# Kernel tuning notes

Hardware: AMD Instinct MI355X
Metric: run time of the kernel (lower is better)

## Reference

```python
import jax, jax.numpy as jnp
import numpy as np

GROUPS = 8   # channels // group_size with group_size=8 for C=64
EPS = 1e-5


def group_norm_qc(x0, x1, gamma, beta):
    """LatticeGroupNorm: stats computed jointly over both cosets per (batch, group)."""
    B, C, H, W = x0.shape
    g = GROUPS
    xg = jnp.concatenate([x0.reshape(B, g, -1), x1.reshape(B, g, -1)], axis=-1)
    mean = xg.mean(axis=-1).reshape(B, g, 1, 1, 1)
    var = xg.var(axis=-1).reshape(B, g, 1, 1, 1)
    inv = jax.lax.rsqrt(var + EPS)
    ga = gamma[None, :, None, None]
    be = beta[None, :, None, None]

    def norm(x):
        xr = x.reshape(B, g, C // g, H, W)
        return ((xr - mean) * inv).reshape(B, C, H, W) * ga + be

    return norm(x0), norm(x1)


def qc_conv(x0, x1, w_center, w_corner, bias):
    """Quincunx LatticePad+LatticeConvolution with stencil
    [(0,0),(2,0),(0,2),(2,2),(1,1)], center (1,1).
    w_center: [O,I] tap (1,1) (same-coset 1x1).
    w_corner: [O,I,2,2] taps (0,0),(2,0),(0,2),(2,2) (cross-coset 2x2).
    Pad keeps output cosets the same size as inputs ('same' lattice conv)."""
    dn = ('NCHW', 'OIHW', 'NCHW')

    def c1(x):
        return jnp.einsum('oi,bihw->bohw', w_center, x)

    def c2(x, pad):
        return jax.lax.conv_general_dilated(x, w_corner, (1, 1), pad,
                                            dimension_numbers=dn)

    b = bias[None, :, None, None]
    # coset0 output gathers coset1 at (i-1+a, j-1+b) -> pad top/left
    out0 = c1(x0) + c2(x1, ((1, 0), (1, 0))) + b
    # coset1 output gathers coset0 at (i+a, j+b) -> pad bottom/right
    out1 = c1(x1) + c2(x0, ((0, 1), (0, 1))) + b
    return out0, out1


def setup_inputs() -> dict:
    key = jax.random.key(0)
    ks = jax.random.split(key, 10)
    B, C, H, W = 2, 64, 256, 256
    s = 0.05
    return {
        'x0': jax.random.normal(ks[0], (B, C, H, W), jnp.float32),
        'x1': jax.random.normal(ks[1], (B, C, H, W), jnp.float32),
        'g1': jnp.ones((C,), jnp.float32),
        'b1': jnp.zeros((C,), jnp.float32),
        'w1_center': jax.random.normal(ks[2], (C, C), jnp.float32) * s,
        'w1_corner': jax.random.normal(ks[3], (C, C, 2, 2), jnp.float32) * s,
        'bias1': jax.random.normal(ks[4], (C,), jnp.float32) * s,
        'g2': jnp.ones((C,), jnp.float32),
        'b2': jnp.zeros((C,), jnp.float32),
        'w2_center': jax.random.normal(ks[5], (C, C), jnp.float32) * s,
        'w2_corner': jax.random.normal(ks[6], (C, C, 2, 2), jnp.float32) * s,
        'bias2': jax.random.normal(ks[7], (C,), jnp.float32) * s,
        'w_skip': jax.random.normal(ks[8], (C, C), jnp.float32) * s,
        'bias_skip': jax.random.normal(ks[9], (C,), jnp.float32) * s,
        'g_skip': jnp.ones((C,), jnp.float32),
        'beta_skip': jnp.zeros((C,), jnp.float32),
    }


def reference(x0, x1, g1, b1, w1_center, w1_corner, bias1,
              g2, b2, w2_center, w2_corner, bias2,
              w_skip, bias_skip, g_skip, beta_skip):
    # conv path: GN -> ReLU -> pad+conv -> GN -> ReLU -> pad+conv
    h0, h1 = group_norm_qc(x0, x1, g1, b1)
    h0, h1 = jax.nn.relu(h0), jax.nn.relu(h1)
    h0, h1 = qc_conv(h0, h1, w1_center, w1_corner, bias1)
    h0, h1 = group_norm_qc(h0, h1, g2, b2)
    h0, h1 = jax.nn.relu(h0), jax.nn.relu(h1)
    h0, h1 = qc_conv(h0, h1, w2_center, w2_corner, bias2)
    # skip path: 1x1 lattice conv (stencil [(0,0)]) -> GN
    bsk = bias_skip[None, :, None, None]
    s0 = jnp.einsum('oi,bihw->bohw', w_skip, x0) + bsk
    s1 = jnp.einsum('oi,bihw->bohw', w_skip, x1) + bsk
    s0, s1 = group_norm_qc(s0, s1, g_skip, beta_skip)
    # residual add; stack the two cosets as leading axis for a single output
    return jnp.stack([h0 + s0, h1 + s1])
```

## Files before the change

### kernel.cpp

```cpp
#include <hip/hip_runtime.h>

typedef __attribute__((ext_vector_type(8))) __bf16 bf16x8;
typedef __attribute__((ext_vector_type(2))) __bf16 bf16x2;
typedef __attribute__((ext_vector_type(4))) float f32x4;

#define MFMA16(a,b,c) __builtin_amdgcn_mfma_f32_16x16x32_bf16(a,b,c,0,0,0)

static constexpr int HW = 65536;
static constexpr int WD = 256;
static constexpr int NB = 2;
static constexpr double INV_N = 1.0 / 1048576.0;
static constexpr float EPSV = 1e-5f;

static constexpr size_t OFF_P1  = 0;
static constexpr size_t OFF_P2  = 131072;
static constexpr size_t OFF_NRM = 196608;
static constexpr size_t OFF_A1  = 200704;
static constexpr size_t OFF_A2  = OFF_A1 + 40960;
static constexpr size_t OFF_XT  = OFF_A2 + 40960;
static constexpr size_t SZ_T    = (size_t)2 * NB * HW * 64 * 2;
static constexpr size_t OFF_S   = OFF_XT + SZ_T;
static constexpr size_t OFF_H   = OFF_S + SZ_T;

__global__ void k_prep(const float* __restrict__ wc1, const float* __restrict__ wk1,
                       const float* __restrict__ wc2, const float* __restrict__ wk2,
                       __bf16* __restrict__ A1, __bf16* __restrict__ A2) {
  const int stage = blockIdx.x;
  const float* wc = stage ? wc2 : wc1;
  const float* wk = stage ? wk2 : wk1;
  __bf16* A = stage ? A2 : A1;
  for (int idx = threadIdx.x; idx < 64 * 320; idx += blockDim.x) {
    int o = idx / 320, k = idx - o * 320;
    float v;
    if (k < 64) v = wc[o * 64 + k];
    else {
      int t = (k - 64) >> 6;
      int c = k & 63;
      v = wk[(o * 64 + c) * 4 + t];
    }
    A[idx] = (__bf16)v;
  }
}

__global__ __launch_bounds__(256) void k1(
    const float* __restrict__ x0, const float* __restrict__ x1,
    const float* __restrict__ wskip, const float* __restrict__ bskip,
    __bf16* __restrict__ xt, __bf16* __restrict__ sout, float* __restrict__ p1) {
  const int row = blockIdx.x;
  const int b   = blockIdx.y;
  const int co  = blockIdx.z;
  const float* x = co ? x1 : x0;
  __shared__ __attribute__((aligned(16))) __bf16 tile[256 * 72];
  __shared__ float redp[64];
  __shared__ float reds[16];
  const int t = threadIdx.x;
  const int wv = t >> 6, lane = t & 63;

  const float* xbase = x + (size_t)b * 64 * HW + (size_t)row * WD + t;
  __bf16* xtbase = xt + (((size_t)(co * NB + b) * HW) + (size_t)row * WD + t) * 64;

  for (int cg = 0; cg < 8; ++cg) {
    bf16x8 v;
    float sum = 0.f, sq = 0.f;
#pragma unroll
    for (int j = 0; j < 8; ++j) {
      float f = xbase[(size_t)(cg * 8 + j) * HW];
      v[j] = (__bf16)f;
      sum += f;
      sq = fmaf(f, f, sq);
    }
    *(bf16x8*)&tile[t * 72 + cg * 8] = v;
    *(bf16x8*)&xtbase[cg * 8] = v;
#pragma unroll
    for (int m = 1; m < 64; m <<= 1) {
      sum += __shfl_xor(sum, m, 64);
      sq  += __shfl_xor(sq, m, 64);
    }
    if (lane == 0) {
      redp[wv * 16 + cg] = sum;
      redp[wv * 16 + 8 + cg] = sq;
    }
  }
  __syncthreads();

  const int ln = lane & 15, q = lane >> 4;
  const int ch0 = wv * 16 + q * 4;
  bf16x8 a0, a1;
#pragma unroll
  for (int j = 0; j < 8; ++j) {
    a0[j] = (__bf16)wskip[(wv * 16 + ln) * 64 + q * 8 + j];
    a1[j] = (__bf16)wskip[(wv * 16 + ln) * 64 + 32 + q * 8 + j];
  }
  float bia[4];
#pragma unroll
  for (int r = 0; r < 4; ++r) bia[r] = bskip[ch0 + r];

  float ssum = 0.f, ssq = 0.f;
  for (int n = 0; n < 16; ++n) {
    f32x4 acc = {0.f, 0.f, 0.f, 0.f};
    bf16x8 b0 = *(const bf16x8*)&tile[(n * 16 + ln) * 72 + q * 8];
    bf16x8 b1 = *(const bf16x8*)&tile[(n * 16 + ln) * 72 + 32 + q * 8];
    acc = MFMA16(a0, b0, acc);
    acc = MFMA16(a1, b1, acc);
    float v[4];
#pragma unroll
    for (int r = 0; r < 4; ++r) {
      v[r] = acc[r] + bia[r];
      ssum += v[r];
      ssq = fmaf(v[r], v[r], ssq);
    }
    size_t sb = (((size_t)(co * NB + b) * HW) + (size_t)row * WD + n * 16 + ln) * 64 + ch0;
    bf16x2 p0; p0[0] = (__bf16)v[0]; p0[1] = (__bf16)v[1];
    bf16x2 p1v; p1v[0] = (__bf16)v[2]; p1v[1] = (__bf16)v[3];
    *(bf16x2*)&sout[sb] = p0;
    *(bf16x2*)&sout[sb + 2] = p1v;
  }
#pragma unroll
  for (int m = 1; m < 32; m <<= 1) {
    ssum += __shfl_xor(ssum, m, 64);
    ssq  += __shfl_xor(ssq, m, 64);
  }
  if (lane == 0)  { reds[2 * wv] = ssum;     reds[8 + 2 * wv] = ssq; }
  if (lane == 32) { reds[2 * wv + 1] = ssum; reds[8 + 2 * wv + 1] = ssq; }

  __syncthreads();
  if (t < 32) {
    float val;
    if (t < 16) val = redp[t] + redp[16 + t] + redp[32 + t] + redp[48 + t];
    else val = reds[t - 16];
    const int bf1 = (co * 2 + b) * 256 + row;
    p1[(size_t)bf1 * 32 + t] = val;
  }
}

__global__ __launch_bounds__(256) void k_r1(
    const float* __restrict__ p1, const float* __restrict__ g1, const float* __restrict__ be1,
    const float* __restrict__ gsk, const float* __restrict__ besk, float* __restrict__ nrm) {
  const int t = threadIdx.x;
  __shared__ double red[64];
  const int sid = t >> 2, sub = t & 3;
  const int which = sid >> 5, b = (sid >> 4) & 1, kg = sid & 15;
  const int col = which * 16 + kg;
  double v = 0.0;
  for (int j = sub; j < 512; j += 4) {
    int co = j >> 8, rr = j & 255;
    v += (double)p1[((size_t)(co * 2 + b) * 256 + rr) * 32 + col];
  }
  v += __shfl_xor(v, 1, 64);
  v += __shfl_xor(v, 2, 64);
  if (sub == 0) red[sid] = v;
  __syncthreads();
  {
    int half = t >> 7;
    int b2 = (t >> 6) & 1, ch = t & 63, g = ch >> 3;
    int base = half * 32 + b2 * 16;
    double mean = red[base + g] * INV_N;
    double var  = red[base + 8 + g] * INV_N - mean * mean;
    float inv  = rsqrtf((float)var + EPSV);
    float ga = half ? gsk[ch] : g1[ch];
    float be = half ? besk[ch] : be1[ch];
    float sc = inv * ga;
    nrm[half * 256 + b2 * 128 + ch] = sc;
    nrm[half * 256 + b2 * 128 + 64 + ch] = be - (float)mean * sc;
  }
}

__global__ __launch_bounds__(256) void k2(
    const __bf16* __restrict__ xt, const __bf16* __restrict__ A1,
    const float* __restrict__ nrm, const float* __restrict__ bias1,
    __bf16* __restrict__ h, float* __restrict__ p2) {
  const int tx = blockIdx.x & 15, ty = blockIdx.x >> 4;
  const int b = blockIdx.y;
  const int y0p = ty * 8, x0p = tx * 16;
  __shared__ __attribute__((aligned(16))) __bf16 tl[2][153 * 72];
  __shared__ float sc[64], sh[64];
  __shared__ float lst[16];
  const int t = threadIdx.x;

  if (t < 64) {
    sc[t] = nrm[b * 128 + t];
    sh[t] = nrm[b * 128 + 64 + t];
  }
  if (t < 16) lst[t] = 0.f;
  __syncthreads();

  for (int u = t; u < 2 * 153 * 8; u += 256) {
    int cs = u / 1224;
    int rr = u - cs * 1224;
    int px = rr >> 3, cg = rr & 7;
    int ly = px / 17, lx = px - ly * 17;
    int gy = y0p + ly - cs, gx = x0p + lx - cs;
    bf16x8 v;
#pragma unroll
    for (int j = 0; j < 8; ++j) v[j] = (__bf16)0.f;
    if ((unsigned)gy < 256u && (unsigned)gx < 256u) {
      bf16x8 raw = *(const bf16x8*)&xt[(((size_t)(cs * NB + b) * WD + gy) * WD + gx) * 64 + cg * 8];
#pragma unroll
      for (int j = 0; j < 8; ++j) {
        float f = fmaf((float)raw[j], sc[cg * 8 + j], sh[cg * 8 + j]);
        v[j] = (__bf16)fmaxf(f, 0.f);
      }
    }
    *(bf16x8*)&tl[cs][px * 72 + cg * 8] = v;
  }
  __syncthreads();

  const int wv = t >> 6, lane = t & 63, ln = lane & 15, q = lane >> 4;
  const int co = wv & 1, mh = wv >> 1;
  const int q8 = q * 8;
  bf16x8 af[2][10];
#pragma unroll
  for (int m = 0; m < 2; ++m)
#pragma unroll
    for (int kk = 0; kk < 10; ++kk)
      af[m][kk] = *(const bf16x8*)&A1[(mh * 32 + m * 16 + ln) * 320 + kk * 32 + q8];

  f32x4 acc[8][2];
#pragma unroll
  for (int n = 0; n < 8; ++n)
#pragma unroll
    for (int m = 0; m < 2; ++m) acc[n][m] = (f32x4){0.f, 0.f, 0.f, 0.f};

  const __bf16* tc = tl[co];
  const __bf16* to = tl[1 - co];
#pragma unroll
  for (int n = 0; n < 8; ++n) {
    const int cpix = co ? ((n + 1) * 17 + ln + 1) : (n * 17 + ln);
    const int tb = n * 17 + ln;
    const __bf16* pc = tc + cpix * 72 + q8;
    const __bf16* p0 = to + tb * 72 + q8;
    const __bf16* p1p = to + (tb + 1) * 72 + q8;
    const __bf16* p2p = to + (tb + 17) * 72 + q8;
    const __bf16* p3 = to + (tb + 18) * 72 + q8;
    bf16x8 bb;
    bb = *(const bf16x8*)pc;         acc[n][0]=MFMA16(af[0][0],bb,acc[n][0]); acc[n][1]=MFMA16(af[1][0],bb,acc[n][1]);
    bb = *(const bf16x8*)(pc + 32);  acc[n][0]=MFMA16(af[0][1],bb,acc[n][0]); acc[n][1]=MFMA16(af[1][1],bb,acc[n][1]);
    bb = *(const bf16x8*)p0;         acc[n][0]=MFMA16(af[0][2],bb,acc[n][0]); acc[n][1]=MFMA16(af[1][2],bb,acc[n][1]);
    bb = *(const bf16x8*)(p0 + 32);  acc[n][0]=MFMA16(af[0][3],bb,acc[n][0]); acc[n][1]=MFMA16(af[1][3],bb,acc[n][1]);
    bb = *(const bf16x8*)p1p;        acc[n][0]=MFMA16(af[0][4],bb,acc[n][0]); acc[n][1]=MFMA16(af[1][4],bb,acc[n][1]);
    bb = *(const bf16x8*)(p1p + 32); acc[n][0]=MFMA16(af[0][5],bb,acc[n][0]); acc[n][1]=MFMA16(af[1][5],bb,acc[n][1]);
    bb = *(const bf16x8*)p2p;        acc[n][0]=MFMA16(af[0][6],bb,acc[n][0]); acc[n][1]=MFMA16(af[1][6],bb,acc[n][1]);
    bb = *(const bf16x8*)(p2p + 32); acc[n][0]=MFMA16(af[0][7],bb,acc[n][0]); acc[n][1]=MFMA16(af[1][7],bb,acc[n][1]);
    bb = *(const bf16x8*)p3;         acc[n][0]=MFMA16(af[0][8],bb,acc[n][0]); acc[n][1]=MFMA16(af[1][8],bb,acc[n][1]);
    bb = *(const bf16x8*)(p3 + 32);  acc[n][0]=MFMA16(af[0][9],bb,acc[n][0]); acc[n][1]=MFMA16(af[1][9],bb,acc[n][1]);
  }

  float s2s[2] = {0.f, 0.f}, s2q[2] = {0.f, 0.f};
  float bia[2][4];
#pragma unroll
  for (int m = 0; m < 2; ++m)
#pragma unroll
    for (int r = 0; r < 4; ++r) bia[m][r] = bias1[mh * 32 + m * 16 + q * 4 + r];

#pragma unroll
  for (int n = 0; n < 8; ++n) {
    int gy = y0p + n;
#pragma unroll
    for (int m = 0; m < 2; ++m) {
      int ch0 = mh * 32 + m * 16 + q * 4;
      size_t hb = (((size_t)(co * NB + b) * WD + gy) * WD + x0p + ln) * 64 + ch0;
      float v[4];
#pragma unroll
      for (int r = 0; r < 4; ++r) {
        v[r] = acc[n][m][r] + bia[m][r];
        s2s[m] += v[r];
        s2q[m] = fmaf(v[r], v[r], s2q[m]);
      }
      bf16x2 p0; p0[0] = (__bf16)v[0]; p0[1] = (__bf16)v[1];
      bf16x2 p1v; p1v[0] = (__bf16)v[2]; p1v[1] = (__bf16)v[3];
      *(bf16x2*)&h[hb] = p0;
      *(bf16x2*)&h[hb + 2] = p1v;
    }
  }
#pragma unroll
  for (int m = 0; m < 2; ++m) {
    float a_ = s2s[m], c_ = s2q[m];
#pragma unroll
    for (int mk = 1; mk < 32; mk <<= 1) {
      a_ += __shfl_xor(a_, mk, 64);
      c_ += __shfl_xor(c_, mk, 64);
    }
    if ((lane & 31) == 0) {
      int g = mh * 4 + m * 2 + (q >> 1);
      atomicAdd(&lst[g], a_);
      atomicAdd(&lst[8 + g], c_);
    }
  }
  __syncthreads();
  if (t < 16) p2[((size_t)b * 512 + blockIdx.x) * 16 + t] = lst[t];
}

__global__ __launch_bounds__(256) void k_r2(
    const float* __restrict__ p2, const float* __restrict__ g2, const float* __restrict__ be2,
    float* __restrict__ nrm) {
  const int t = threadIdx.x;
  __shared__ double red[32];
  const int sid = t >> 3, sub = t & 7;
  const int b = sid >> 4, col = sid & 15;
  double v = 0.0;
  for (int j = sub; j < 512; j += 8)
    v += (double)p2[((size_t)b * 512 + j) * 16 + col];
  v += __shfl_xor(v, 1, 64);
  v += __shfl_xor(v, 2, 64);
  v += __shfl_xor(v, 4, 64);
  if (sub == 0) red[sid] = v;
  __syncthreads();
  if (t < 128) {
    int b2 = t >> 6, ch = t & 63, g = ch >> 3;
    double mean = red[b2 * 16 + g] * INV_N;
    double var  = red[b2 * 16 + 8 + g] * INV_N - mean * mean;
    float inv  = rsqrtf((float)var + EPSV);
    float sc = inv * g2[ch];
    nrm[512 + b2 * 128 + ch] = sc;
    nrm[512 + b2 * 128 + 64 + ch] = be2[ch] - (float)mean * sc;
  }
}

__global__ __launch_bounds__(256) void k3(
    const __bf16* __restrict__ hin, const __bf16* __restrict__ A2,
    const float* __restrict__ nrm, const float* __restrict__ bias2,
    const __bf16* __restrict__ sin_, float* __restrict__ out) {
  const int tx = blockIdx.x & 15, ty = blockIdx.x >> 4;
  const int b = blockIdx.y;
  const int y0p = ty * 8, x0p = tx * 16;
  __shared__ __attribute__((aligned(16))) __bf16 tl[2][153 * 72];
  __shared__ float sc2[64], sh2[64], scS[64], shS[64];
  const int t = threadIdx.x;

  if (t < 64) {
    sc2[t] = nrm[512 + b * 128 + t];
    sh2[t] = nrm[512 + b * 128 + 64 + t];
    scS[t] = nrm[256 + b * 128 + t];
    shS[t] = nrm[256 + b * 128 + 64 + t];
  }
  __syncthreads();

  for (int u = t; u < 2 * 153 * 8; u += 256) {
    int cs = u / 1224;
    int rr = u - cs * 1224;
    int px = rr >> 3, cg = rr & 7;
    int ly = px / 17, lx = px - ly * 17;
    int gy = y0p + ly - cs, gx = x0p + lx - cs;
    bf16x8 v;
#pragma unroll
    for (int j = 0; j < 8; ++j) v[j] = (__bf16)0.f;
    if ((unsigned)gy < 256u && (unsigned)gx < 256u) {
      bf16x8 raw = *(const bf16x8*)&hin[(((size_t)(cs * NB + b) * WD + gy) * WD + gx) * 64 + cg * 8];
#pragma unroll
      for (int j = 0; j < 8; ++j) {
        float f = fmaf((float)raw[j], sc2[cg * 8 + j], sh2[cg * 8 + j]);
        v[j] = (__bf16)fmaxf(f, 0.f);
      }
    }
    *(bf16x8*)&tl[cs][px * 72 + cg * 8] = v;
  }
  __syncthreads();

  const int wv = t >> 6, lane = t & 63, ln = lane & 15, q = lane >> 4;
  const int co = wv & 1, mh = wv >> 1;
  const int q8 = q * 8;
  bf16x8 af[2][10];
#pragma unroll
  for (int m = 0; m < 2; ++m)
#pragma unroll
    for (int kk = 0; kk < 10; ++kk)
      af[m][kk] = *(const bf16x8*)&A2[(mh * 32 + m * 16 + ln) * 320 + kk * 32 + q8];

  f32x4 acc[8][2];
#pragma unroll
  for (int n = 0; n < 8; ++n)
#pragma unroll
    for (int m = 0; m < 2; ++m) acc[n][m] = (f32x4){0.f, 0.f, 0.f, 0.f};

  const __bf16* tc = tl[co];
  const __bf16* to = tl[1 - co];
#pragma unroll
  for (int n = 0; n < 8; ++n) {
    const int cpix = co ? ((n + 1) * 17 + ln + 1) : (n * 17 + ln);
    const int tb = n * 17 + ln;
    const __bf16* pc = tc + cpix * 72 + q8;
    const __bf16* p0 = to + tb * 72 + q8;
    const __bf16* p1p = to + (tb + 1) * 72 + q8;
    const __bf16* p2p = to + (tb + 17) * 72 + q8;
    const __bf16* p3 = to + (tb + 18) * 72 + q8;
    bf16x8 bb;
    bb = *(const bf16x8*)pc;         acc[n][0]=MFMA16(af[0][0],bb,acc[n][0]); acc[n][1]=MFMA16(af[1][0],bb,acc[n][1]);
    bb = *(const bf16x8*)(pc + 32);  acc[n][0]=MFMA16(af[0][1],bb,acc[n][0]); acc[n][1]=MFMA16(af[1][1],bb,acc[n][1]);
    bb = *(const bf16x8*)p0;         acc[n][0]=MFMA16(af[0][2],bb,acc[n][0]); acc[n][1]=MFMA16(af[1][2],bb,acc[n][1]);
    bb = *(const bf16x8*)(p0 + 32);  acc[n][0]=MFMA16(af[0][3],bb,acc[n][0]); acc[n][1]=MFMA16(af[1][3],bb,acc[n][1]);
    bb = *(const bf16x8*)p1p;        acc[n][0]=MFMA16(af[0][4],bb,acc[n][0]); acc[n][1]=MFMA16(af[1][4],bb,acc[n][1]);
    bb = *(const bf16x8*)(p1p + 32); acc[n][0]=MFMA16(af[0][5],bb,acc[n][0]); acc[n][1]=MFMA16(af[1][5],bb,acc[n][1]);
    bb = *(const bf16x8*)p2p;        acc[n][0]=MFMA16(af[0][6],bb,acc[n][0]); acc[n][1]=MFMA16(af[1][6],bb,acc[n][1]);
    bb = *(const bf16x8*)(p2p + 32); acc[n][0]=MFMA16(af[0][7],bb,acc[n][0]); acc[n][1]=MFMA16(af[1][7],bb,acc[n][1]);
    bb = *(const bf16x8*)p3;         acc[n][0]=MFMA16(af[0][8],bb,acc[n][0]); acc[n][1]=MFMA16(af[1][8],bb,acc[n][1]);
    bb = *(const bf16x8*)(p3 + 32);  acc[n][0]=MFMA16(af[0][9],bb,acc[n][0]); acc[n][1]=MFMA16(af[1][9],bb,acc[n][1]);
  }

  float bia[2][4], sA[2][4], sB[2][4];
#pragma unroll
  for (int m = 0; m < 2; ++m)
#pragma unroll
    for (int r = 0; r < 4; ++r) {
      int ch = mh * 32 + m * 16 + q * 4 + r;
      bia[m][r] = bias2[ch];
      sA[m][r] = scS[ch];
      sB[m][r] = shS[ch];
    }

#pragma unroll
  for (int n = 0; n < 8; ++n) {
    int gy = y0p + n;
#pragma unroll
    for (int m = 0; m < 2; ++m) {
      int ch0 = mh * 32 + m * 16 + q * 4;
      size_t sb = (((size_t)(co * NB + b) * WD + gy) * WD + x0p + ln) * 64 + ch0;
      bf16x2 sv0 = *(const bf16x2*)&sin_[sb];
      bf16x2 sv1 = *(const bf16x2*)&sin_[sb + 2];
      float sraw[4] = {(float)sv0[0], (float)sv0[1], (float)sv1[0], (float)sv1[1]};
      size_t ob = ((size_t)(co * NB + b) * 64 + ch0) * HW + (size_t)gy * WD + x0p + ln;
#pragma unroll
      for (int r = 0; r < 4; ++r) {
        float v = acc[n][m][r] + bia[m][r] + fmaf(sraw[r], sA[m][r], sB[m][r]);
        out[ob + (size_t)r * HW] = v;
      }
    }
  }
}

extern "C" void kernel_launch(void* const* d_in, const int* in_sizes, int n_in,
                              void* d_out, int out_size, void* d_ws, size_t ws_size,
                              hipStream_t stream) {
  (void)in_sizes; (void)n_in; (void)out_size; (void)ws_size;
  const float* x0    = (const float*)d_in[0];
  const float* x1    = (const float*)d_in[1];
  const float* g1    = (const float*)d_in[2];
  const float* b1    = (const float*)d_in[3];
  const float* w1c   = (const float*)d_in[4];
  const float* w1k   = (const float*)d_in[5];
  const float* bias1 = (const float*)d_in[6];
  const float* g2    = (const float*)d_in[7];
  const float* b2    = (const float*)d_in[8];
  const float* w2c   = (const float*)d_in[9];
  const float* w2k   = (const float*)d_in[10];
  const float* bias2 = (const float*)d_in[11];
  const float* wsk   = (const float*)d_in[12];
  const float* bsk   = (const float*)d_in[13];
  const float* gsk   = (const float*)d_in[14];
  const float* besk  = (const float*)d_in[15];

  char* ws = (char*)d_ws;
  float*  p1 = (float*)(ws + OFF_P1);
  float*  p2 = (float*)(ws + OFF_P2);
  float*  nrm = (float*)(ws + OFF_NRM);
  __bf16* A1 = (__bf16*)(ws + OFF_A1);
  __bf16* A2 = (__bf16*)(ws + OFF_A2);
  __bf16* xt = (__bf16*)(ws + OFF_XT);
  __bf16* s  = (__bf16*)(ws + OFF_S);
  __bf16* h  = (__bf16*)(ws + OFF_H);

  k_prep<<<2, 256, 0, stream>>>(w1c, w1k, w2c, w2k, A1, A2);
  k1<<<dim3(256, 2, 2), 256, 0, stream>>>(x0, x1, wsk, bsk, xt, s, p1);
  k_r1<<<1, 256, 0, stream>>>(p1, g1, b1, gsk, besk, nrm);
  k2<<<dim3(512, 2), 256, 0, stream>>>(xt, A1, nrm, bias1, h, p2);
  k_r2<<<1, 256, 0, stream>>>(p2, g2, b2, nrm);
  k3<<<dim3(512, 2), 256, 0, stream>>>(h, A2, nrm, bias2, s, (float*)d_out);
}
```

Before: 329.4 us.

## Coalesce intermediate stores via LDS staging and fragment-native skip layout, swizzle blocks

The skip-path intermediate is now stored in a layout that matches the MFMA fragment order, so each lane writes and later reads one contiguous bf16x4 instead of two scattered bf16x2 accesses. In k2 the conv output is staged through the reused shared tile and written back as 16-byte rows, which coalesces the global h writes. Block indices in k2 and k3 are remapped so neighbouring launched blocks cover different tile rows, aiming for better cache and channel locality. The cost is an extra LDS round trip and barriers in k2, plus a tightly coupled layout contract between the skip producer and k3.

New measurement: 328.2 us. No clear change (-0.4%).

```diff
diff --git a/kernel.cpp b/kernel.cpp
--- a/kernel.cpp
+++ b/kernel.cpp
@@ -1,6 +1,7 @@
 #include <hip/hip_runtime.h>
 
 typedef __attribute__((ext_vector_type(8))) __bf16 bf16x8;
+typedef __attribute__((ext_vector_type(4))) __bf16 bf16x4;
 typedef __attribute__((ext_vector_type(2))) __bf16 bf16x2;
 typedef __attribute__((ext_vector_type(4))) float f32x4;
 
@@ -102,18 +103,17 @@
     bf16x8 b1 = *(const bf16x8*)&tile[(n * 16 + ln) * 72 + 32 + q * 8];
     acc = MFMA16(a0, b0, acc);
     acc = MFMA16(a1, b1, acc);
+    bf16x4 sv;
     float v[4];
 #pragma unroll
     for (int r = 0; r < 4; ++r) {
       v[r] = acc[r] + bia[r];
       ssum += v[r];
       ssq = fmaf(v[r], v[r], ssq);
-    }
-    size_t sb = (((size_t)(co * NB + b) * HW) + (size_t)row * WD + n * 16 + ln) * 64 + ch0;
-    bf16x2 p0; p0[0] = (__bf16)v[0]; p0[1] = (__bf16)v[1];
-    bf16x2 p1v; p1v[0] = (__bf16)v[2]; p1v[1] = (__bf16)v[3];
-    *(bf16x2*)&sout[sb] = p0;
-    *(bf16x2*)&sout[sb + 2] = p1v;
+      sv[r] = (__bf16)v[r];
+    }
+    size_t sb = ((size_t)(co * NB + b) * 4096 + row * 16 + n) * 1024 + (wv * 4 + q) * 64 + ln * 4;
+    *(bf16x4*)&sout[sb] = sv;
   }
 #pragma unroll
   for (int m = 1; m < 32; m <<= 1) {
@@ -169,7 +169,8 @@
     const __bf16* __restrict__ xt, const __bf16* __restrict__ A1,
     const float* __restrict__ nrm, const float* __restrict__ bias1,
     __bf16* __restrict__ h, float* __restrict__ p2) {
-  const int tx = blockIdx.x & 15, ty = blockIdx.x >> 4;
+  const int blk = ((blockIdx.x & 7) << 6) | (blockIdx.x >> 3);
+  const int tx = blk & 15, ty = blk >> 4;
   const int b = blockIdx.y;
   const int y0p = ty * 8, x0p = tx * 16;
   __shared__ __attribute__((aligned(16))) __bf16 tl[2][153 * 72];
@@ -245,6 +246,8 @@
     bb = *(const bf16x8*)(p3 + 32);  acc[n][0]=MFMA16(af[0][9],bb,acc[n][0]); acc[n][1]=MFMA16(af[1][9],bb,acc[n][1]);
   }
 
+  __syncthreads();
+
   float s2s[2] = {0.f, 0.f}, s2q[2] = {0.f, 0.f};
   float bia[2][4];
 #pragma unroll
@@ -253,25 +256,20 @@
     for (int r = 0; r < 4; ++r) bia[m][r] = bias1[mh * 32 + m * 16 + q * 4 + r];
 
 #pragma unroll
-  for (int n = 0; n < 8; ++n) {
-    int gy = y0p + n;
+  for (int n = 0; n < 8; ++n)
 #pragma unroll
     for (int m = 0; m < 2; ++m) {
-      int ch0 = mh * 32 + m * 16 + q * 4;
-      size_t hb = (((size_t)(co * NB + b) * WD + gy) * WD + x0p + ln) * 64 + ch0;
-      float v[4];
+      bf16x4 hv;
 #pragma unroll
       for (int r = 0; r < 4; ++r) {
-        v[r] = acc[n][m][r] + bia[m][r];
-        s2s[m] += v[r];
-        s2q[m] = fmaf(v[r], v[r], s2q[m]);
+        float v = acc[n][m][r] + bia[m][r];
+        s2s[m] += v;
+        s2q[m] = fmaf(v, v, s2q[m]);
+        hv[r] = (__bf16)v;
       }
-      bf16x2 p0; p0[0] = (__bf16)v[0]; p0[1] = (__bf16)v[1];
-      bf16x2 p1v; p1v[0] = (__bf16)v[2]; p1v[1] = (__bf16)v[3];
-      *(bf16x2*)&h[hb] = p0;
-      *(bf16x2*)&h[hb + 2] = p1v;
-    }
-  }
+      *(bf16x4*)&tl[co][(n * 16 + ln) * 72 + mh * 32 + m * 16 + q * 4] = hv;
+    }
+
 #pragma unroll
   for (int m = 0; m < 2; ++m) {
     float a_ = s2s[m], c_ = s2q[m];
@@ -287,6 +285,16 @@
     }
   }
   __syncthreads();
+
+  for (int i = 0; i < 8; ++i) {
+    int co2 = i >> 2;
+    int idx = (i & 3) * 256 + t;
+    int px = idx >> 3, chunk = idx & 7;
+    int gy = y0p + (px >> 4), gx = x0p + (px & 15);
+    bf16x8 vv = *(const bf16x8*)&tl[co2][px * 72 + chunk * 8];
+    *(bf16x8*)&h[(((size_t)(co2 * NB + b) * WD + gy) * WD + gx) * 64 + chunk * 8] = vv;
+  }
+
   if (t < 16) p2[((size_t)b * 512 + blockIdx.x) * 16 + t] = lst[t];
 }
 
@@ -320,7 +328,8 @@
     const __bf16* __restrict__ hin, const __bf16* __restrict__ A2,
     const float* __restrict__ nrm, const float* __restrict__ bias2,
     const __bf16* __restrict__ sin_, float* __restrict__ out) {
-  const int tx = blockIdx.x & 15, ty = blockIdx.x >> 4;
+  const int blk = ((blockIdx.x & 7) << 6) | (blockIdx.x >> 3);
+  const int tx = blk & 15, ty = blk >> 4;
   const int b = blockIdx.y;
   const int y0p = ty * 8, x0p = tx * 16;
   __shared__ __attribute__((aligned(16))) __bf16 tl[2][153 * 72];
@@ -413,14 +422,12 @@
 #pragma unroll
     for (int m = 0; m < 2; ++m) {
       int ch0 = mh * 32 + m * 16 + q * 4;
-      size_t sb = (((size_t)(co * NB + b) * WD + gy) * WD + x0p + ln) * 64 + ch0;
-      bf16x2 sv0 = *(const bf16x2*)&sin_[sb];
-      bf16x2 sv1 = *(const bf16x2*)&sin_[sb + 2];
-      float sraw[4] = {(float)sv0[0], (float)sv0[1], (float)sv1[0], (float)sv1[1]};
+      size_t sb = ((size_t)(co * NB + b) * 4096 + gy * 16 + tx) * 1024 + (mh * 8 + m * 4 + q) * 64 + ln * 4;
+      bf16x4 sv = *(const bf16x4*)&sin_[sb];
       size_t ob = ((size_t)(co * NB + b) * 64 + ch0) * HW + (size_t)gy * WD + x0p + ln;
 #pragma unroll
       for (int r = 0; r < 4; ++r) {
-        float v = acc[n][m][r] + bia[m][r] + fmaf(sraw[r], sA[m][r], sB[m][r]);
+        float v = acc[n][m][r] + bia[m][r] + fmaf((float)sv[r], sA[m][r], sB[m][r]);
         out[ob + (size_t)r * HW] = v;
       }
     }
```
